# Kernel optimization log

Hardware: AMD Instinct MI355X
Metric: run time of the kernel (lower is better)

Reference implementation:

```python
import jax, jax.numpy as jnp
import numpy as np

B, C, H, W = 2, 256, 64, 64
HEADS, SR = 8, 4
D = C // HEADS          # head dim = 32
N = H * W               # query length = 4096
EPS = 1e-5


def _conv(x, w, stride=1, pad=0, groups=1, b=None):
    out = jax.lax.conv_general_dilated(
        x, w, (stride, stride), [(pad, pad), (pad, pad)],
        dimension_numbers=('NCHW', 'OIHW', 'NCHW'),
        feature_group_count=groups)
    if b is not None:
        out = out + b[None, :, None, None]
    return out


def _bn(x, p):
    # p: [4, C] = (gamma, beta, running_mean, running_var), eval-mode BN
    g, b, m, v = p[0], p[1], p[2], p[3]
    s = g / jnp.sqrt(v + EPS)
    return (x - m[None, :, None, None]) * s[None, :, None, None] + b[None, :, None, None]


def setup_inputs() -> dict:
    key = jax.random.key(0)
    ks = iter(jax.random.split(key, 32))
    nrm = lambda shape, s=0.05: jax.random.normal(next(ks), shape, jnp.float32) * s
    def bnp():
        return jnp.stack([jnp.ones((C,), jnp.float32), jnp.zeros((C,), jnp.float32),
                          jax.random.normal(next(ks), (C,), jnp.float32) * 0.1,
                          jax.random.uniform(next(ks), (C,), jnp.float32) + 0.5])
    return dict(
        x=jax.random.normal(next(ks), (B, C, H, W), jnp.float32),
        relative_pos_enc=jax.random.normal(next(ks), (B, 2, 64, 64), jnp.float32),
        q_w=nrm((C, C, 1, 1)), q_b=jnp.zeros((C,), jnp.float32),
        kv_w=nrm((2 * C, C, 1, 1)), kv_b=jnp.zeros((2 * C,), jnp.float32),
        sr1_dw_w=nrm((C, 1, SR + 3, SR + 3)), sr1_bn1=bnp(),
        sr1_pw_w=nrm((C, 1, 1, 1), 0.5), sr1_bn2=bnp(),
        sr2_dw_w=nrm((C, 1, SR // 2 + 3, SR // 2 + 3)), sr2_bn1=bnp(),
        sr2_pw_w=nrm((C, 1, 1, 1), 0.5), sr2_bn2=bnp(),
        local_w=nrm((C, 1, 3, 3)), local_b=jnp.zeros((C,), jnp.float32),
    )


def reference(x, relative_pos_enc, q_w, q_b, kv_w, kv_b,
              sr1_dw_w, sr1_bn1, sr1_pw_w, sr1_bn2,
              sr2_dw_w, sr2_bn1, sr2_pw_w, sr2_bn2,
              local_w, local_b):
    scale = D ** -0.5
    # q: 1x1 conv -> [B, heads, N, D]; both branches use the FIRST half of heads
    q = _conv(x, q_w, b=q_b).reshape(B, HEADS, D, N).transpose(0, 1, 3, 2)
    qh = q[:, :HEADS // 2]

    def branch(dw_w, bn1, pw_w, bn2, stride, pad, rpe_slice):
        # SR path: depthwise conv + BN + ReLU, depthwise 1x1 + BN
        y = jax.nn.relu(_bn(_conv(x, dw_w, stride, pad, groups=C), bn1))
        y = _bn(_conv(y, pw_w, groups=C), bn2)
        # local 3x3 depthwise mixing with residual
        y = _conv(y, local_w, pad=1, groups=C, b=local_b) + y
        kv = _conv(y, kv_w, b=kv_b)                # [B, 2C, h', w']
        k, v = jnp.split(kv, 2, axis=1)
        L = 2 * y.shape[2] * y.shape[3]            # channel-fold doubles kv length
        k = k.reshape(B, HEADS // 2, D, L)
        v = v.reshape(B, HEADS // 2, D, L).transpose(0, 1, 3, 2)
        attn = jnp.einsum('bhnd,bhdl->bhnl', qh, k) * scale
        rpe = jax.image.resize(rpe_slice, (B, 1, N, L), method='bicubic')
        attn = jax.nn.softmax(attn + rpe, axis=-1)
        return jnp.einsum('bhnl,bhld->bhnd', attn, v)

    x1 = branch(sr1_dw_w, sr1_bn1, sr1_pw_w, sr1_bn2,
                SR, (SR + 3) // 2, relative_pos_enc[:, 0:1])
    x2 = branch(sr2_dw_w, sr2_bn1, sr2_pw_w, sr2_bn2,
                SR // 2, (SR // 2 + 3) // 2, relative_pos_enc[:, 1:2])
    out = jnp.concatenate([x1, x2], axis=-1)       # [B, heads//2, N, 2D]
    return out.reshape(B, C, H, W)
```

## Files before the change

kernel.cpp:

```cpp
#include <hip/hip_runtime.h>
#include <hip/hip_bf16.h>
#include <math.h>

#define NB 2
#define NC 256
#define HWIN 4096
#define NN 4096
#define ND 32
#define NHH 4
#define EPSV 1e-5f

typedef short short8 __attribute__((ext_vector_type(8)));
typedef float f32x4 __attribute__((ext_vector_type(4)));
typedef unsigned short u16;
typedef unsigned int u32;

#define OFF_T1   0
#define OFF_T2   262144
#define OFF_Q    1310720
#define OFF_KT1  1835008
#define OFF_VT1  1900544
#define OFF_KT2  1966080
#define OFF_VT2  2228224
#define OFF_RCT1 2490368
#define OFF_RCT2 2531328
#define OFF_WT   2695168
#define OFF_PO   2826240
#define OFF_PS   4923392
#define OFF_QWT  5054464

#define QSCALE 0.2550437314857726f
#define LOG2E  1.4426950408889634f

__device__ __forceinline__ u16 f2bf(float x) {
  unsigned u = __float_as_uint(x);
  u += 0x7fffu + ((u >> 16) & 1u);
  return (u16)(u >> 16);
}

__device__ __forceinline__ u32 pk_bf16(float a, float b) {
  __hip_bfloat162 h = __float22bfloat162_rn(make_float2(a, b));
  u32 r; __builtin_memcpy(&r, &h, 4);
  return r;
}

__device__ __forceinline__ float keysw(float t) {
  t = fabsf(t);
  float w;
  if (t < 1.f)       w = ((1.5f*t - 2.5f)*t)*t + 1.f;
  else if (t < 2.f)  w = ((-0.5f*t + 2.5f)*t - 4.f)*t + 2.f;
  else               w = 0.f;
  return w;
}

template<int KS, int STR, int PAD, int OH>
__device__ __forceinline__ void dwconv_body(int idx, const float* __restrict__ x,
    const float* __restrict__ dww, const float* __restrict__ bn1,
    const float* __restrict__ pww, const float* __restrict__ bn2,
    float* __restrict__ tout) {
  const int hw = OH*OH;
  int s = idx % hw; int c = (idx/hw) % NC; int b = idx/(hw*NC);
  int oy = s / OH, ox = s % OH;
  const float* xp = x + (b*NC + c)*HWIN;
  const float* wp = dww + c*KS*KS;
  float acc = 0.f;
  #pragma unroll
  for (int ky = 0; ky < KS; ++ky) {
    int iy = oy*STR - PAD + ky;
    if (iy < 0 || iy >= 64) continue;
    #pragma unroll
    for (int kx = 0; kx < KS; ++kx) {
      int ix = ox*STR - PAD + kx;
      if (ix < 0 || ix >= 64) continue;
      acc += xp[iy*64 + ix] * wp[ky*KS + kx];
    }
  }
  float s1 = bn1[c] * rsqrtf(bn1[3*NC + c] + EPSV);
  float z = (acc - bn1[2*NC + c])*s1 + bn1[NC + c];
  z = fmaxf(z, 0.f);
  float s2 = bn2[c] * rsqrtf(bn2[3*NC + c] + EPSV);
  z = z * (pww[c]*s2) + (bn2[NC + c] - bn2[2*NC + c]*s2);
  tout[idx] = z;
}

__device__ __forceinline__ void rpe_body(int idx, const float* __restrict__ rpe,
                                         u16* __restrict__ rcT, int L, int ch) {
  int r = idx & 63; int l = (idx >> 6) % L; int b = idx / (64*L);
  float f = ((float)l + 0.5f)*(64.f/(float)L) - 0.5f;
  int i0 = (int)floorf(f) - 1;
  const float* rp = rpe + ((b*2 + ch)*64 + r)*64;
  float v = 0.f, wsum = 0.f;
  #pragma unroll
  for (int j = 0; j < 4; ++j) {
    int i = i0 + j;
    if (i >= 0 && i < 64) {
      float w = keysw(f - (float)i);
      v += w * rp[i]; wsum += w;
    }
  }
  rcT[((size_t)(b*L + l))*80 + 4 + r] = f2bf(v / wsum);
}

__global__ void __launch_bounds__(256) prep_kernel(
    const float* __restrict__ x,
    const float* __restrict__ dw1, const float* __restrict__ bn11,
    const float* __restrict__ pw1, const float* __restrict__ bn12, float* __restrict__ t1,
    const float* __restrict__ dw2, const float* __restrict__ bn21,
    const float* __restrict__ pw2, const float* __restrict__ bn22, float* __restrict__ t2,
    const float* __restrict__ rpe, u16* __restrict__ rct1, u16* __restrict__ rct2,
    const float* __restrict__ kvw, float* __restrict__ wt,
    const float* __restrict__ qw, float* __restrict__ qwt) {
  int blk = blockIdx.x;
  int t = threadIdx.x;
  if (blk < 512) {
    dwconv_body<7,4,3,16>(blk*256 + t, x, dw1, bn11, pw1, bn12, t1);
  } else if (blk < 2560) {
    dwconv_body<5,2,2,32>((blk-512)*256 + t, x, dw2, bn21, pw2, bn22, t2);
  } else if (blk < 2816) {
    rpe_body((blk-2560)*256 + t, rpe, rct1, 512, 0);
  } else if (blk < 3840) {
    rpe_body((blk-2816)*256 + t, rpe, rct2, 2048, 1);
  } else if (blk < 3968) {
    int base = ((blk-3840)*256 + t)*4;
    float4 vv = *(const float4*)(kvw + base);
    int o = base >> 8, c = base & 255;
    wt[(c+0)*512 + o] = vv.x;
    wt[(c+1)*512 + o] = vv.y;
    wt[(c+2)*512 + o] = vv.z;
    wt[(c+3)*512 + o] = vv.w;
  } else {
    int base = ((blk-3968)*256 + t)*4;
    float4 vv = *(const float4*)(qw + base);
    int oc = base >> 8, c = base & 255;
    qwt[(c+0)*128 + oc] = vv.x;
    qwt[(c+1)*128 + oc] = vv.y;
    qwt[(c+2)*128 + oc] = vv.z;
    qwt[(c+3)*128 + oc] = vv.w;
  }
}

__global__ void __launch_bounds__(256) localkv_kernel(
    const float* __restrict__ t1in, const float* __restrict__ t2in,
    const float* __restrict__ lw, const float* __restrict__ lb,
    const float* __restrict__ wt, const float* __restrict__ kvb,
    u16* __restrict__ kt1, u16* __restrict__ vt1,
    u16* __restrict__ kt2, u16* __restrict__ vt2,
    const float* __restrict__ x, const float* __restrict__ qwt,
    const float* __restrict__ qb, u16* __restrict__ q) {
  __shared__ float sbuf[NC*16];
  int blk = blockIdx.x, tid = threadIdx.x;
  if (blk < 320) {
    const float* tin; u16 *kT, *vT; int OH, hw, b, s0;
    if (blk < 64) { tin = t1in; kT = kt1; vT = vt1; OH = 16; hw = 256;  b = blk >> 5;  s0 = (blk & 31)*8; }
    else { int v = blk-64; tin = t2in; kT = kt2; vT = vt2; OH = 32; hw = 1024; b = v >> 7; s0 = (v & 127)*8; }
    int oy = s0 / OH, ox0 = s0 % OH;
    int ci = tid >> 3, i = tid & 7;
    int ox = ox0 + i;
    #pragma unroll
    for (int p = 0; p < 8; ++p) {
      int c = p*32 + ci;
      const float* tp = tin + (b*NC + c)*hw;
      const float* wp = lw + c*9;
      float acc = lb[c];
      #pragma unroll
      for (int dy = 0; dy < 3; ++dy) {
        int iy = oy + dy - 1;
        if (iy < 0 || iy >= OH) continue;
        #pragma unroll
        for (int dx = 0; dx < 3; ++dx) {
          int ix = ox + dx - 1;
          if (ix < 0 || ix >= OH) continue;
          acc += tp[iy*OH + ix]*wp[dy*3 + dx];
        }
      }
      acc += tp[oy*OH + ox];
      sbuf[c*12 + i] = acc;
    }
    __syncthreads();
    float acc0[8], acc1[8];
    float b0 = kvb[tid], b1 = kvb[tid + 256];
    #pragma unroll
    for (int j = 0; j < 8; ++j) { acc0[j] = b0; acc1[j] = b1; }
    #pragma unroll 4
    for (int c = 0; c < NC; ++c) {
      f32x4 ya = *(const f32x4*)(sbuf + c*12);
      f32x4 yb = *(const f32x4*)(sbuf + c*12 + 4);
      float w0 = wt[c*512 + tid];
      float w1 = wt[c*512 + tid + 256];
      #pragma unroll
      for (int j = 0; j < 4; ++j) {
        acc0[j]   += w0*ya[j];  acc0[4+j] += w0*yb[j];
        acc1[j]   += w1*ya[j];  acc1[4+j] += w1*yb[j];
      }
    }
    int hh2 = tid >> 6, r = tid & 63, d = r >> 1, e = r & 1;
    int L = 2*hw;
    u16* kp = kT + ((size_t)((b*NHH + hh2)*L + e*hw + s0))*ND + d;
    #pragma unroll
    for (int j = 0; j < 8; ++j) kp[j*ND] = f2bf(acc0[j]);
    u16* vp = vT + ((size_t)((b*NHH + hh2)*ND + d))*L + e*hw + s0;
    #pragma unroll
    for (int j = 0; j < 8; ++j) vp[j] = f2bf(acc1[j]);
  } else {
    int blk2 = blk - 320;
    int b = blk2 >> 8;
    int n0 = (blk2 & 255) * 16;
    #pragma unroll
    for (int j = 0; j < 16; ++j) {
      int idx = tid + 256*j;
      int c = idx >> 4, i = idx & 15;
      sbuf[idx] = x[(b*NC + c)*HWIN + n0 + i];
    }
    __syncthreads();
    int half = tid >> 7, oc = tid & 127;
    float bias = qb[oc];
    float acc[8];
    #pragma unroll
    for (int i = 0; i < 8; ++i) acc[i] = bias;
    #pragma unroll 4
    for (int c = 0; c < NC; ++c) {
      float w = qwt[c*128 + oc];
      #pragma unroll
      for (int i = 0; i < 8; ++i) acc[i] += w * sbuf[c*16 + half*8 + i];
    }
    int h = oc >> 5, d = oc & 31;
    u16* qp = q + (((size_t)(b*NHH + h))*NN + n0 + half*8)*ND + d;
    #pragma unroll
    for (int i = 0; i < 8; ++i) qp[i*ND] = f2bf(acc[i]*QSCALE);
  }
}

__global__ void __launch_bounds__(256) attn_kernel(
    const u16* __restrict__ qbf,
    const u16* __restrict__ kt1, const u16* __restrict__ vt1, const u16* __restrict__ rct1,
    const u16* __restrict__ kt2, const u16* __restrict__ vt2, const u16* __restrict__ rct2,
    u32* __restrict__ po32, float* __restrict__ ps,
    float* __restrict__ out) {
  __shared__ u16 kbuf[64*72];
  __shared__ u16 vbuf[32*72];
  __shared__ u32 pbuf_all[4][16*36];
  int u = blockIdx.x;
  int br, b, hh, rb, chunk;
  if (u < 512) { br = 0; b = u >> 8; hh = (u >> 6) & 3; rb = u & 63; chunk = 0; }
  else { int v = u - 512; br = 1; chunk = v & 3; rb = (v >> 2) & 63; hh = (v >> 8) & 3; b = v >> 10; }
  int L = br ? 2048 : 512;
  const u16* kT  = br ? kt2 : kt1;
  const u16* vT  = br ? vt2 : vt1;
  const u16* rcT = br ? rct2 : rct1;
  int l0base = chunk * 512;
  int tid = threadIdx.x;
  int w = tid >> 6, lane = tid & 63;
  int g = lane >> 4, lo = lane & 15;
  u32* pbuf = pbuf_all[w];
  u16* pbuf16 = (u16*)pbuf;
  int n = rb*64 + w*16 + lo;

  const u16* kbase = kT + (size_t)(b*NHH + hh)*L*ND;
  const u16* vbase = vT + (size_t)(b*NHH + hh)*ND*L;
  const u16* rcTb  = rcT + (size_t)b*L*80;

  short8 qf = *(const short8*)(qbf + (((size_t)(b*NHH + hh))*NN + n)*ND + 8*g);

  float fr = ((float)n + 0.5f)*(1.f/64.f) - 0.5f;
  int ri0 = (int)floorf(fr) - 1;
  int a = (w < 2) ? rb - 2 : rb - 1;
  int rmin = a & ~3;
  float wr4[4]; float wsum = 0.f;
  #pragma unroll
  for (int j = 0; j < 4; ++j) {
    int i = ri0 + j;
    float wv = (i >= 0 && i < 64) ? keysw(fr - (float)i) : 0.f;
    wr4[j] = wv; wsum += wv;
  }
  float invw = LOG2E / wsum;
  float wt8[8];
  #pragma unroll
  for (int s = 0; s < 8; ++s) {
    float acc = 0.f;
    #pragma unroll
    for (int j = 0; j < 4; ++j)
      acc += (ri0 + j - rmin == s) ? wr4[j]*invw : 0.f;
    wt8[s] = acc;
  }
  short8 wtf;
  {
    u32 p0 = pk_bf16(wt8[0], wt8[1]), p1 = pk_bf16(wt8[2], wt8[3]);
    u32 p2 = pk_bf16(wt8[4], wt8[5]), p3 = pk_bf16(wt8[6], wt8[7]);
    uint4 uu = make_uint4(p0, p1, p2, p3);
    wtf = __builtin_bit_cast(short8, uu);
    if (g != 0) wtf = (short8)0;
  }
  const u16* rcrow0 = rcTb + (rmin + 4);

  const f32x4 zero = {0.f, 0.f, 0.f, 0.f};
  float ssum = 0.f;
  f32x4 o0 = zero, o1 = zero;

  int kr_row = tid >> 2, kr_col = (tid & 3)*8;
  int vr_row = tid >> 3, vr_col = (tid & 7)*8;

  auto stageLoad = [&](short8& kr, short8& vr, int l0) {
    kr = *(const short8*)(kbase + (size_t)(l0 + kr_row)*ND + kr_col);
    vr = *(const short8*)(vbase + (size_t)vr_row*L + l0 + vr_col);
  };
  auto stageStore = [&](short8 kr, short8 vr) {
    *(short8*)(kbuf + kr_row*72 + kr_col) = kr;
    *(short8*)(vbuf + vr_row*72 + vr_col) = vr;
  };
  auto loadRC = [&](uint4 (&rc)[4], int l0) {
    #pragma unroll
    for (int c = 0; c < 4; ++c) {
      const u16* arow = rcrow0 + (size_t)(l0 + 16*c + lo)*80;
      uint2 ra = *(const uint2*)arow;
      uint2 rb2 = *(const uint2*)(arow + 4);
      rc[c] = make_uint4(ra.x, ra.y, rb2.x, rb2.y);
    }
  };

  short8 kr, vr;
  uint4 rcA[4], rcB[4];
  stageLoad(kr, vr, l0base);
  loadRC(rcA, l0base);

  for (int t = 0; t < 8; ++t) {
    stageStore(kr, vr);
    __syncthreads();
    if (t < 7) { stageLoad(kr, vr, l0base + (t+1)*64); loadRC(rcB, l0base + (t+1)*64); }
    f32x4 s4[4];
    #pragma unroll
    for (int c = 0; c < 4; ++c) {
      short8 rcf = __builtin_bit_cast(short8, rcA[c]);
      f32x4 accr = __builtin_amdgcn_mfma_f32_16x16x32_bf16(rcf, wtf, zero, 0, 0, 0);
      short8 kf = *(const short8*)(kbuf + (16*c + lo)*72 + 8*g);
      s4[c] = __builtin_amdgcn_mfma_f32_16x16x32_bf16(kf, qf, accr, 0, 0, 0);
    }
    float psum = 0.f;
    u32 pk[8];
    #pragma unroll
    for (int c = 0; c < 4; ++c) {
      float p0 = exp2f(s4[c][0]), p1 = exp2f(s4[c][1]);
      float p2 = exp2f(s4[c][2]), p3 = exp2f(s4[c][3]);
      psum += (p0 + p1) + (p2 + p3);
      pk[2*c]   = pk_bf16(p0, p1);
      pk[2*c+1] = pk_bf16(p2, p3);
    }
    ssum += psum;
    #pragma unroll
    for (int c = 0; c < 4; ++c)
      *(uint2*)(pbuf + lo*36 + 8*c + 2*g) = make_uint2(pk[2*c], pk[2*c+1]);
    short8 pf0 = *(const short8*)(pbuf16 + lo*72 + 8*g);
    short8 pf1 = *(const short8*)(pbuf16 + lo*72 + 32 + 8*g);
    short8 v00 = *(const short8*)(vbuf + lo*72 + 8*g);
    short8 v01 = *(const short8*)(vbuf + lo*72 + 32 + 8*g);
    short8 v10 = *(const short8*)(vbuf + (16+lo)*72 + 8*g);
    short8 v11 = *(const short8*)(vbuf + (16+lo)*72 + 32 + 8*g);
    o0 = __builtin_amdgcn_mfma_f32_16x16x32_bf16(v00, pf0, o0, 0, 0, 0);
    o1 = __builtin_amdgcn_mfma_f32_16x16x32_bf16(v10, pf0, o1, 0, 0, 0);
    o0 = __builtin_amdgcn_mfma_f32_16x16x32_bf16(v01, pf1, o0, 0, 0, 0);
    o1 = __builtin_amdgcn_mfma_f32_16x16x32_bf16(v11, pf1, o1, 0, 0, 0);
    if (t < 7) {
      #pragma unroll
      for (int j = 0; j < 4; ++j) rcA[j] = rcB[j];
    }
    __syncthreads();
  }

  ssum += __shfl_xor(ssum, 16, 64);
  ssum += __shfl_xor(ssum, 32, 64);
  if (br == 0) {
    float inv = 1.f/ssum;
    f32x4 w0 = o0*inv, w1 = o1*inv;
    float* op = out + ((size_t)((b*NC + hh*64 + rb)*64 + (w*16 + lo)))*64;
    *(f32x4*)(op + 4*g)      = w0;
    *(f32x4*)(op + 16 + 4*g) = w1;
  } else {
    int bh = b*NHH + hh;
    int row = bh*NN + n;
    u32* pop = po32 + ((size_t)chunk*32768 + row)*16;
    pop[2*g]     = pk_bf16(o0[0], o0[1]);
    pop[2*g + 1] = pk_bf16(o0[2], o0[3]);
    pop[8 + 2*g]     = pk_bf16(o1[0], o1[1]);
    pop[8 + 2*g + 1] = pk_bf16(o1[2], o1[3]);
    if (g == 0) ps[(size_t)chunk*32768 + row] = ssum;
  }
}

__global__ void __launch_bounds__(256) combine_kernel(
    const u32* __restrict__ po32, const float* __restrict__ ps,
    float* __restrict__ out) {
  int gid = blockIdx.x*256 + threadIdx.x;
  int row = gid >> 2, part = gid & 3;
  float sden = ps[row] + ps[32768 + row] + ps[65536 + row] + ps[98304 + row];
  float inv = 1.f/sden;
  float o[8];
  #pragma unroll
  for (int i = 0; i < 8; ++i) o[i] = 0.f;
  #pragma unroll
  for (int chunk = 0; chunk < 4; ++chunk) {
    const u32* pp = po32 + ((size_t)chunk*32768 + row)*16 + part*4;
    uint4 a = *(const uint4*)pp;
    u32 av[4] = {a.x, a.y, a.z, a.w};
    #pragma unroll
    for (int j = 0; j < 4; ++j) {
      o[2*j]   += __uint_as_float(av[j] << 16);
      o[2*j+1] += __uint_as_float(av[j] & 0xffff0000u);
    }
  }
  int bh = row >> 12, n = row & 4095;
  float* op = out + ((size_t)(((bh>>2)*NC + (bh&3)*64 + (n>>6))*64 + (n&63)))*64 + 32 + part*8;
  #pragma unroll
  for (int j = 0; j < 2; ++j) {
    f32x4 v = {o[4*j]*inv, o[4*j+1]*inv, o[4*j+2]*inv, o[4*j+3]*inv};
    *(f32x4*)(op + 4*j) = v;
  }
}

extern "C" void kernel_launch(void* const* d_in, const int* in_sizes, int n_in,
                              void* d_out, int out_size, void* d_ws, size_t ws_size,
                              hipStream_t stream) {
  const float* x    = (const float*)d_in[0];
  const float* rpe  = (const float*)d_in[1];
  const float* qw   = (const float*)d_in[2];
  const float* qb   = (const float*)d_in[3];
  const float* kvw  = (const float*)d_in[4];
  const float* kvb  = (const float*)d_in[5];
  const float* dw1  = (const float*)d_in[6];
  const float* bn11 = (const float*)d_in[7];
  const float* pw1  = (const float*)d_in[8];
  const float* bn12 = (const float*)d_in[9];
  const float* dw2  = (const float*)d_in[10];
  const float* bn21 = (const float*)d_in[11];
  const float* pw2  = (const float*)d_in[12];
  const float* bn22 = (const float*)d_in[13];
  const float* lw   = (const float*)d_in[14];
  const float* lb   = (const float*)d_in[15];
  float* out = (float*)d_out;
  float* ws  = (float*)d_ws;

  float* t1   = ws + OFF_T1;
  float* t2   = ws + OFF_T2;
  u16*   q    = (u16*)(ws + OFF_Q);
  u16*   kt1  = (u16*)(ws + OFF_KT1);
  u16*   vt1  = (u16*)(ws + OFF_VT1);
  u16*   kt2  = (u16*)(ws + OFF_KT2);
  u16*   vt2  = (u16*)(ws + OFF_VT2);
  u16*   rct1 = (u16*)(ws + OFF_RCT1);
  u16*   rct2 = (u16*)(ws + OFF_RCT2);
  float* wt   = ws + OFF_WT;
  u32*   po32 = (u32*)(ws + OFF_PO);
  float* ps   = ws + OFF_PS;
  float* qwt  = ws + OFF_QWT;

  hipLaunchKernelGGL(prep_kernel, dim3(4000), dim3(256), 0, stream,
                     x, dw1, bn11, pw1, bn12, t1, dw2, bn21, pw2, bn22, t2,
                     rpe, rct1, rct2, kvw, wt, qw, qwt);
  hipLaunchKernelGGL(localkv_kernel, dim3(832), dim3(256), 0, stream,
                     t1, t2, lw, lb, wt, kvb, kt1, vt1, kt2, vt2, x, qwt, qb, q);
  hipLaunchKernelGGL(attn_kernel, dim3(2560), dim3(256), 0, stream,
                     q, kt1, vt1, rct1, kt2, vt2, rct2, po32, ps, out);
  hipLaunchKernelGGL(combine_kernel, dim3(512), dim3(256), 0, stream,
                     po32, ps, out);
}
```

Measured before the change: 191.7 us.

## Read K/V fragments directly from global in tiled V layout, drop LDS staging

```diff
diff --git a/kernel.cpp b/kernel.cpp
--- a/kernel.cpp
+++ b/kernel.cpp
@@ -198,7 +198,8 @@
     u16* kp = kT + ((size_t)((b*NHH + hh2)*L + e*hw + s0))*ND + d;
     #pragma unroll
     for (int j = 0; j < 8; ++j) kp[j*ND] = f2bf(acc0[j]);
-    u16* vp = vT + ((size_t)((b*NHH + hh2)*ND + d))*L + e*hw + s0;
+    int l0v = e*hw + s0;
+    u16* vp = vT + ((size_t)((b*NHH + hh2)*(L/64) + (l0v >> 6))*ND + d)*64 + (l0v & 63);
     #pragma unroll
     for (int j = 0; j < 8; ++j) vp[j] = f2bf(acc1[j]);
   } else {
@@ -230,14 +231,12 @@
   }
 }
 
-__global__ void __launch_bounds__(256) attn_kernel(
+__global__ void __launch_bounds__(256, 6) attn_kernel(
     const u16* __restrict__ qbf,
     const u16* __restrict__ kt1, const u16* __restrict__ vt1, const u16* __restrict__ rct1,
     const u16* __restrict__ kt2, const u16* __restrict__ vt2, const u16* __restrict__ rct2,
     u32* __restrict__ po32, float* __restrict__ ps,
     float* __restrict__ out) {
-  __shared__ u16 kbuf[64*72];
-  __shared__ u16 vbuf[32*72];
   __shared__ u32 pbuf_all[4][16*36];
   int u = blockIdx.x;
   int br, b, hh, rb, chunk;
@@ -296,50 +295,33 @@
   float ssum = 0.f;
   f32x4 o0 = zero, o1 = zero;
 
-  int kr_row = tid >> 2, kr_col = (tid & 3)*8;
-  int vr_row = tid >> 3, vr_col = (tid & 7)*8;
-
-  auto stageLoad = [&](short8& kr, short8& vr, int l0) {
-    kr = *(const short8*)(kbase + (size_t)(l0 + kr_row)*ND + kr_col);
-    vr = *(const short8*)(vbase + (size_t)vr_row*L + l0 + vr_col);
-  };
-  auto stageStore = [&](short8 kr, short8 vr) {
-    *(short8*)(kbuf + kr_row*72 + kr_col) = kr;
-    *(short8*)(vbuf + vr_row*72 + vr_col) = vr;
-  };
-  auto loadRC = [&](uint4 (&rc)[4], int l0) {
+  for (int t = 0; t < 8; ++t) {
+    int l0 = l0base + t*64;
+    const u16* ktile = kbase + (size_t)l0*ND;
+    f32x4 s4[4];
     #pragma unroll
     for (int c = 0; c < 4; ++c) {
       const u16* arow = rcrow0 + (size_t)(l0 + 16*c + lo)*80;
       uint2 ra = *(const uint2*)arow;
       uint2 rb2 = *(const uint2*)(arow + 4);
-      rc[c] = make_uint4(ra.x, ra.y, rb2.x, rb2.y);
-    }
-  };
-
-  short8 kr, vr;
-  uint4 rcA[4], rcB[4];
-  stageLoad(kr, vr, l0base);
-  loadRC(rcA, l0base);
-
-  for (int t = 0; t < 8; ++t) {
-    stageStore(kr, vr);
-    __syncthreads();
-    if (t < 7) { stageLoad(kr, vr, l0base + (t+1)*64); loadRC(rcB, l0base + (t+1)*64); }
-    f32x4 s4[4];
-    #pragma unroll
-    for (int c = 0; c < 4; ++c) {
-      short8 rcf = __builtin_bit_cast(short8, rcA[c]);
+      short8 rcf = __builtin_bit_cast(short8, make_uint4(ra.x, ra.y, rb2.x, rb2.y));
       f32x4 accr = __builtin_amdgcn_mfma_f32_16x16x32_bf16(rcf, wtf, zero, 0, 0, 0);
-      short8 kf = *(const short8*)(kbuf + (16*c + lo)*72 + 8*g);
+      short8 kf = *(const short8*)(ktile + (16*c + lo)*ND + 8*g);
       s4[c] = __builtin_amdgcn_mfma_f32_16x16x32_bf16(kf, qf, accr, 0, 0, 0);
     }
+    const u16* vtile = vbase + (size_t)(l0 >> 6)*(ND*64);
+    short8 v00 = *(const short8*)(vtile + lo*64 + 8*g);
+    short8 v01 = *(const short8*)(vtile + lo*64 + 32 + 8*g);
+    short8 v10 = *(const short8*)(vtile + (16 + lo)*64 + 8*g);
+    short8 v11 = *(const short8*)(vtile + (16 + lo)*64 + 32 + 8*g);
     float psum = 0.f;
     u32 pk[8];
     #pragma unroll
     for (int c = 0; c < 4; ++c) {
-      float p0 = exp2f(s4[c][0]), p1 = exp2f(s4[c][1]);
-      float p2 = exp2f(s4[c][2]), p3 = exp2f(s4[c][3]);
+      float p0 = __builtin_amdgcn_exp2f(s4[c][0]);
+      float p1 = __builtin_amdgcn_exp2f(s4[c][1]);
+      float p2 = __builtin_amdgcn_exp2f(s4[c][2]);
+      float p3 = __builtin_amdgcn_exp2f(s4[c][3]);
       psum += (p0 + p1) + (p2 + p3);
       pk[2*c]   = pk_bf16(p0, p1);
       pk[2*c+1] = pk_bf16(p2, p3);
@@ -350,19 +332,10 @@
       *(uint2*)(pbuf + lo*36 + 8*c + 2*g) = make_uint2(pk[2*c], pk[2*c+1]);
     short8 pf0 = *(const short8*)(pbuf16 + lo*72 + 8*g);
     short8 pf1 = *(const short8*)(pbuf16 + lo*72 + 32 + 8*g);
-    short8 v00 = *(const short8*)(vbuf + lo*72 + 8*g);
-    short8 v01 = *(const short8*)(vbuf + lo*72 + 32 + 8*g);
-    short8 v10 = *(const short8*)(vbuf + (16+lo)*72 + 8*g);
-    short8 v11 = *(const short8*)(vbuf + (16+lo)*72 + 32 + 8*g);
     o0 = __builtin_amdgcn_mfma_f32_16x16x32_bf16(v00, pf0, o0, 0, 0, 0);
     o1 = __builtin_amdgcn_mfma_f32_16x16x32_bf16(v10, pf0, o1, 0, 0, 0);
     o0 = __builtin_amdgcn_mfma_f32_16x16x32_bf16(v01, pf1, o0, 0, 0, 0);
     o1 = __builtin_amdgcn_mfma_f32_16x16x32_bf16(v11, pf1, o1, 0, 0, 0);
-    if (t < 7) {
-      #pragma unroll
-      for (int j = 0; j < 4; ++j) rcA[j] = rcB[j];
-    }
-    __syncthreads();
   }
 
   ssum += __shfl_xor(ssum, 16, 64);
```

Result: slower. 217.1 us (+13.2%).

## Tile V layout in 64-column blocks, XOR-swizzle LDS buffers, use native exp2

Applied to the files above, without the earlier changes.

```diff
diff --git a/kernel.cpp b/kernel.cpp
--- a/kernel.cpp
+++ b/kernel.cpp
@@ -198,7 +198,8 @@
     u16* kp = kT + ((size_t)((b*NHH + hh2)*L + e*hw + s0))*ND + d;
     #pragma unroll
     for (int j = 0; j < 8; ++j) kp[j*ND] = f2bf(acc0[j]);
-    u16* vp = vT + ((size_t)((b*NHH + hh2)*ND + d))*L + e*hw + s0;
+    int l0v = e*hw + s0;
+    u16* vp = vT + ((size_t)((b*NHH + hh2)*(L/64) + (l0v >> 6))*ND + d)*64 + (l0v & 63);
     #pragma unroll
     for (int j = 0; j < 8; ++j) vp[j] = f2bf(acc1[j]);
   } else {
@@ -236,9 +237,9 @@
     const u16* __restrict__ kt2, const u16* __restrict__ vt2, const u16* __restrict__ rct2,
     u32* __restrict__ po32, float* __restrict__ ps,
     float* __restrict__ out) {
-  __shared__ u16 kbuf[64*72];
-  __shared__ u16 vbuf[32*72];
-  __shared__ u32 pbuf_all[4][16*36];
+  __shared__ u16 kbuf[64*32];
+  __shared__ u16 vbuf[32*64];
+  __shared__ u32 pbuf_all[4][16*32];
   int u = blockIdx.x;
   int br, b, hh, rb, chunk;
   if (u < 512) { br = 0; b = u >> 8; hh = (u >> 6) & 3; rb = u & 63; chunk = 0; }
@@ -297,15 +298,21 @@
   f32x4 o0 = zero, o1 = zero;
 
   int kr_row = tid >> 2, kr_col = (tid & 3)*8;
+  int kr_sw  = ((kr_row >> 1) & 3)*8;
   int vr_row = tid >> 3, vr_col = (tid & 7)*8;
+  int vr_sw  = (vr_row & 7)*8;
+  int ksw = ((lo >> 1) & 3)*8;
+  int vsw = (lo & 7)*8;
+  int psw4 = (lo & 7)*4;
+  int psw8 = (lo & 7)*8;
 
   auto stageLoad = [&](short8& kr, short8& vr, int l0) {
     kr = *(const short8*)(kbase + (size_t)(l0 + kr_row)*ND + kr_col);
-    vr = *(const short8*)(vbase + (size_t)vr_row*L + l0 + vr_col);
+    vr = *(const short8*)(vbase + (size_t)(l0 >> 6)*(ND*64) + vr_row*64 + vr_col);
   };
   auto stageStore = [&](short8 kr, short8 vr) {
-    *(short8*)(kbuf + kr_row*72 + kr_col) = kr;
-    *(short8*)(vbuf + vr_row*72 + vr_col) = vr;
+    *(short8*)(kbuf + kr_row*32 + (kr_col ^ kr_sw)) = kr;
+    *(short8*)(vbuf + vr_row*64 + (vr_col ^ vr_sw)) = vr;
   };
   auto loadRC = [&](uint4 (&rc)[4], int l0) {
     #pragma unroll
@@ -331,15 +338,17 @@
     for (int c = 0; c < 4; ++c) {
       short8 rcf = __builtin_bit_cast(short8, rcA[c]);
       f32x4 accr = __builtin_amdgcn_mfma_f32_16x16x32_bf16(rcf, wtf, zero, 0, 0, 0);
-      short8 kf = *(const short8*)(kbuf + (16*c + lo)*72 + 8*g);
+      short8 kf = *(const short8*)(kbuf + (16*c + lo)*32 + ((8*g) ^ ksw));
       s4[c] = __builtin_amdgcn_mfma_f32_16x16x32_bf16(kf, qf, accr, 0, 0, 0);
     }
     float psum = 0.f;
     u32 pk[8];
     #pragma unroll
     for (int c = 0; c < 4; ++c) {
-      float p0 = exp2f(s4[c][0]), p1 = exp2f(s4[c][1]);
-      float p2 = exp2f(s4[c][2]), p3 = exp2f(s4[c][3]);
+      float p0 = __builtin_amdgcn_exp2f(s4[c][0]);
+      float p1 = __builtin_amdgcn_exp2f(s4[c][1]);
+      float p2 = __builtin_amdgcn_exp2f(s4[c][2]);
+      float p3 = __builtin_amdgcn_exp2f(s4[c][3]);
       psum += (p0 + p1) + (p2 + p3);
       pk[2*c]   = pk_bf16(p0, p1);
       pk[2*c+1] = pk_bf16(p2, p3);
@@ -347,13 +356,13 @@
     ssum += psum;
     #pragma unroll
     for (int c = 0; c < 4; ++c)
-      *(uint2*)(pbuf + lo*36 + 8*c + 2*g) = make_uint2(pk[2*c], pk[2*c+1]);
-    short8 pf0 = *(const short8*)(pbuf16 + lo*72 + 8*g);
-    short8 pf1 = *(const short8*)(pbuf16 + lo*72 + 32 + 8*g);
-    short8 v00 = *(const short8*)(vbuf + lo*72 + 8*g);
-    short8 v01 = *(const short8*)(vbuf + lo*72 + 32 + 8*g);
-    short8 v10 = *(const short8*)(vbuf + (16+lo)*72 + 8*g);
-    short8 v11 = *(const short8*)(vbuf + (16+lo)*72 + 32 + 8*g);
+      *(uint2*)(pbuf + lo*32 + ((8*c + 2*g) ^ psw4)) = make_uint2(pk[2*c], pk[2*c+1]);
+    short8 pf0 = *(const short8*)(pbuf16 + lo*64 + ((8*g) ^ psw8));
+    short8 pf1 = *(const short8*)(pbuf16 + lo*64 + ((32 + 8*g) ^ psw8));
+    short8 v00 = *(const short8*)(vbuf + lo*64 + ((8*g) ^ vsw));
+    short8 v01 = *(const short8*)(vbuf + lo*64 + ((32 + 8*g) ^ vsw));
+    short8 v10 = *(const short8*)(vbuf + (16 + lo)*64 + ((8*g) ^ vsw));
+    short8 v11 = *(const short8*)(vbuf + (16 + lo)*64 + ((32 + 8*g) ^ vsw));
     o0 = __builtin_amdgcn_mfma_f32_16x16x32_bf16(v00, pf0, o0, 0, 0, 0);
     o1 = __builtin_amdgcn_mfma_f32_16x16x32_bf16(v10, pf0, o1, 0, 0, 0);
     o0 = __builtin_amdgcn_mfma_f32_16x16x32_bf16(v01, pf1, o0, 0, 0, 0);
```

Result: faster. 183.3 us (-4.4%).
